# Kernel optimization log

Measured on AMD Instinct MI355X. Metric: run time of the kernel, lower is better.

The kernel has to match this reference:

```python
import jax, jax.numpy as jnp
import numpy as np

NEG_INF = -1.0e9  # matches torch masked_fill value


def setup_inputs() -> dict:
    key = jax.random.key(0)
    k1, k2, k3, k4 = jax.random.split(key, 4)
    B, S, H = 32, 4096, 1024
    query = jax.random.normal(k1, (B, 1, H), dtype=jnp.float32)
    keys = jax.random.normal(k2, (B, S, H), dtype=jnp.float32)
    src_mask = jax.random.randint(k3, (B, S), 0, 2) == 1
    # nn.Linear weight [out,in]; y = x @ W.T
    W_query = jax.random.normal(k4, (H, H), dtype=jnp.float32) * (1.0 / np.sqrt(H))
    return {"query": query, "keys": keys, "src_mask": src_mask, "W_query": W_query}


def reference(query, keys, src_mask, W_query):
    # projected query: [B,1,H] @ W.T -> [B,1,H]
    q = jnp.einsum("bqh,oh->bqo", query, W_query)
    # scores: [B,S] (single query squeezed)
    scores = jnp.einsum("bqh,bsh->bqs", q, keys)[:, 0, :]
    scores = jnp.where(src_mask, NEG_INF, scores)
    weights = jax.nn.softmax(scores, axis=-1)[:, None, :]  # [B,1,S]
    context = jnp.einsum("bqs,bsh->bqh", weights, keys)    # [B,1,H]
    return (context, weights)
```

## Files before the change

### kernel.cpp

```cpp
#include <hip/hip_runtime.h>
#include <math.h>

#define BB 32
#define SS 4096
#define HH 1024
#define NCHUNK 32
#define CHUNK (SS / NCHUNK)
#define NEG_INF9 (-1.0e9f)

__device__ __forceinline__ float wave_reduce_sum(float v) {
#pragma unroll
    for (int off = 32; off > 0; off >>= 1) v += __shfl_xor(v, off, 64);
    return v;
}

__device__ __forceinline__ void wave_reduce_sum2(float& a, float& b) {
#pragma unroll
    for (int off = 32; off > 0; off >>= 1) {
        const float ta = __shfl_xor(a, off, 64);
        const float tb = __shfl_xor(b, off, 64);
        a += ta;
        b += tb;
    }
}

__global__ __launch_bounds__(256) void qproj_kernel(const float* __restrict__ query,
                                                    const float* __restrict__ W,
                                                    float* __restrict__ q) {
    const int b    = blockIdx.y;
    const int wave = threadIdx.x >> 6;
    const int lane = threadIdx.x & 63;

    const float4* qp = (const float4*)(query + (size_t)b * HH);
    float4 qv[4];
#pragma unroll
    for (int r = 0; r < 4; ++r) qv[r] = qp[r * 64 + lane];

    const int obase = blockIdx.x * 64 + wave * 16;
    for (int i = 0; i < 16; ++i) {
        const int o = obase + i;
        const float4* wp = (const float4*)(W + (size_t)o * HH);
        float acc = 0.f;
#pragma unroll
        for (int r = 0; r < 4; ++r) {
            const float4 wv = wp[r * 64 + lane];
            acc += wv.x * qv[r].x + wv.y * qv[r].y + wv.z * qv[r].z + wv.w * qv[r].w;
        }
        acc = wave_reduce_sum(acc);
        if (lane == 0) q[(size_t)b * HH + o] = acc;
    }
}

__global__ __launch_bounds__(256) void attn_chunk_kernel(const float* __restrict__ q,
                                                         const float* __restrict__ keys,
                                                         const int* __restrict__ mask,
                                                         float* __restrict__ raw_scores,
                                                         float* __restrict__ pm,
                                                         float* __restrict__ pl,
                                                         float* __restrict__ pO) {
    const int b    = blockIdx.y;
    const int c    = blockIdx.x;
    const int wave = threadIdx.x >> 6;
    const int lane = threadIdx.x & 63;

    const float4* qp = (const float4*)(q + (size_t)b * HH);
    float4 qv[4];
#pragma unroll
    for (int r = 0; r < 4; ++r) qv[r] = qp[r * 64 + lane];

    float m = -INFINITY;
    float l = 0.f;
    float4 acc[4];
#pragma unroll
    for (int r = 0; r < 4; ++r) acc[r] = make_float4(0.f, 0.f, 0.f, 0.f);

    const size_t bbase = (size_t)b * SS;
    const int s0 = c * CHUNK + wave * 2;

#pragma unroll 4
    for (int i = 0; i < CHUNK / 8; ++i) {
        const int s = s0 + 8 * i;
        const float4* kp0 = (const float4*)(keys + (bbase + s) * HH);
        const float4* kp1 = (const float4*)(keys + (bbase + s + 1) * HH);
        float4 kva[4], kvb[4];
#pragma unroll
        for (int r = 0; r < 4; ++r) { kva[r] = kp0[r * 64 + lane]; kvb[r] = kp1[r * 64 + lane]; }

        float sc0 = 0.f, sc1 = 0.f;
#pragma unroll
        for (int r = 0; r < 4; ++r) {
            sc0 += kva[r].x * qv[r].x + kva[r].y * qv[r].y + kva[r].z * qv[r].z + kva[r].w * qv[r].w;
            sc1 += kvb[r].x * qv[r].x + kvb[r].y * qv[r].y + kvb[r].z * qv[r].z + kvb[r].w * qv[r].w;
        }
        wave_reduce_sum2(sc0, sc1);

        const int2 mk = *(const int2*)(mask + bbase + s);
        if (mk.x != 0) sc0 = NEG_INF9;
        if (mk.y != 0) sc1 = NEG_INF9;
        if (lane == 0) *(float2*)(raw_scores + bbase + s) = make_float2(sc0, sc1);

        const float mnew  = fmaxf(m, fmaxf(sc0, sc1));
        const float scale = __expf(m - mnew);
        const float p0    = __expf(sc0 - mnew);
        const float p1    = __expf(sc1 - mnew);
        l = l * scale + p0 + p1;
#pragma unroll
        for (int r = 0; r < 4; ++r) {
            acc[r].x = acc[r].x * scale + p0 * kva[r].x + p1 * kvb[r].x;
            acc[r].y = acc[r].y * scale + p0 * kva[r].y + p1 * kvb[r].y;
            acc[r].z = acc[r].z * scale + p0 * kva[r].z + p1 * kvb[r].z;
            acc[r].w = acc[r].w * scale + p0 * kva[r].w + p1 * kvb[r].w;
        }
        m = mnew;
    }

    __shared__ float  sm[4];
    __shared__ float  sl[4];
    __shared__ float4 sO[4][256];
#pragma unroll
    for (int r = 0; r < 4; ++r) sO[wave][r * 64 + lane] = acc[r];
    if (lane == 0) { sm[wave] = m; sl[wave] = l; }
    __syncthreads();

    const float M = fmaxf(fmaxf(sm[0], sm[1]), fmaxf(sm[2], sm[3]));
    float f[4];
#pragma unroll
    for (int w = 0; w < 4; ++w) f[w] = __expf(sm[w] - M);
    const float L = sl[0] * f[0] + sl[1] * f[1] + sl[2] * f[2] + sl[3] * f[3];

    const int tid = threadIdx.x;
    float4 o = make_float4(0.f, 0.f, 0.f, 0.f);
#pragma unroll
    for (int w = 0; w < 4; ++w) {
        const float4 v = sO[w][tid];
        o.x += f[w] * v.x; o.y += f[w] * v.y; o.z += f[w] * v.z; o.w += f[w] * v.w;
    }
    ((float4*)(pO + ((size_t)b * NCHUNK + c) * HH))[tid] = o;
    if (tid == 0) { pm[b * NCHUNK + c] = M; pl[b * NCHUNK + c] = L; }
}

__global__ __launch_bounds__(256) void combine_kernel(const float* __restrict__ pm,
                                                      const float* __restrict__ pl,
                                                      const float* __restrict__ pO,
                                                      float* __restrict__ context,
                                                      float* __restrict__ weights) {
    const int b   = blockIdx.x;
    const int tid = threadIdx.x;

    float M = -INFINITY;
#pragma unroll
    for (int c = 0; c < NCHUNK; ++c) M = fmaxf(M, pm[b * NCHUNK + c]);
    float fc[NCHUNK];
    float L = 0.f;
#pragma unroll
    for (int c = 0; c < NCHUNK; ++c) {
        fc[c] = __expf(pm[b * NCHUNK + c] - M);
        L += pl[b * NCHUNK + c] * fc[c];
    }
    const float invL = 1.f / L;

    float4 o = make_float4(0.f, 0.f, 0.f, 0.f);
#pragma unroll
    for (int c = 0; c < NCHUNK; ++c) {
        const float4 v = ((const float4*)(pO + ((size_t)b * NCHUNK + c) * HH))[tid];
        const float g = fc[c] * invL;
        o.x += g * v.x; o.y += g * v.y; o.z += g * v.z; o.w += g * v.w;
    }
    ((float4*)(context + (size_t)b * HH))[tid] = o;

    for (int s = tid; s < SS; s += 256) {
        const float sc = weights[(size_t)b * SS + s];
        weights[(size_t)b * SS + s] = __expf(sc - M) * invL;
    }
}

extern "C" void kernel_launch(void* const* d_in, const int* in_sizes, int n_in,
                              void* d_out, int out_size, void* d_ws, size_t ws_size,
                              hipStream_t stream) {
    const float* query = (const float*)d_in[0];
    const float* keys  = (const float*)d_in[1];
    const int*   mask  = (const int*)d_in[2];
    const float* W     = (const float*)d_in[3];

    float* context = (float*)d_out;
    float* weights = (float*)d_out + (size_t)BB * HH;

    float* q  = (float*)d_ws;
    float* pm = q + (size_t)BB * HH;
    float* pl = pm + BB * NCHUNK;
    float* pO = pl + BB * NCHUNK;

    qproj_kernel<<<dim3(HH / 64, BB), 256, 0, stream>>>(query, W, q);
    attn_chunk_kernel<<<dim3(NCHUNK, BB), 256, 0, stream>>>(q, keys, mask, weights, pm, pl, pO);
    combine_kernel<<<BB, 256, 0, stream>>>(pm, pl, pO, context, weights);
}
```

Baseline: 708.1 us.

## Double-buffer key loads, DPP reductions, more chunks, split combine kernel

The attention kernel now register double-buffers the next pair of key rows and mask values while computing the current pair, and skips the accumulator rescale when the running max does not change. Wave reductions use DPP row operations plus readlane instead of shuffle chains. The chunk count doubles, giving more blocks to fill the GPU, and the combine kernel is split across four blocks per batch to parallelise the context and weight normalisation. The cost is higher register pressure from the double buffer and a larger partial-output workspace. The loop is also fully unrolled.

```diff
diff --git a/kernel.cpp b/kernel.cpp
--- a/kernel.cpp
+++ b/kernel.cpp
@@ -4,24 +4,26 @@
 #define BB 32
 #define SS 4096
 #define HH 1024
-#define NCHUNK 32
+#define NCHUNK 64
 #define CHUNK (SS / NCHUNK)
+#define NSPLIT 4
 #define NEG_INF9 (-1.0e9f)
 
-__device__ __forceinline__ float wave_reduce_sum(float v) {
-#pragma unroll
-    for (int off = 32; off > 0; off >>= 1) v += __shfl_xor(v, off, 64);
-    return v;
-}
-
-__device__ __forceinline__ void wave_reduce_sum2(float& a, float& b) {
-#pragma unroll
-    for (int off = 32; off > 0; off >>= 1) {
-        const float ta = __shfl_xor(a, off, 64);
-        const float tb = __shfl_xor(b, off, 64);
-        a += ta;
-        b += tb;
-    }
+__device__ __forceinline__ float dpp_allreduce_add(float x) {
+    int t;
+    t = __builtin_amdgcn_update_dpp(0, __float_as_int(x), 0x111, 0xf, 0xf, false);
+    x += __int_as_float(t);
+    t = __builtin_amdgcn_update_dpp(0, __float_as_int(x), 0x112, 0xf, 0xf, false);
+    x += __int_as_float(t);
+    t = __builtin_amdgcn_update_dpp(0, __float_as_int(x), 0x114, 0xf, 0xf, false);
+    x += __int_as_float(t);
+    t = __builtin_amdgcn_update_dpp(0, __float_as_int(x), 0x118, 0xf, 0xf, false);
+    x += __int_as_float(t);
+    t = __builtin_amdgcn_update_dpp(0, __float_as_int(x), 0x142, 0xf, 0xf, false);
+    x += __int_as_float(t);
+    t = __builtin_amdgcn_update_dpp(0, __float_as_int(x), 0x143, 0xf, 0xf, false);
+    x += __int_as_float(t);
+    return __int_as_float(__builtin_amdgcn_readlane(__float_as_int(x), 63));
 }
 
 __global__ __launch_bounds__(256) void qproj_kernel(const float* __restrict__ query,
@@ -46,8 +48,8 @@
             const float4 wv = wp[r * 64 + lane];
             acc += wv.x * qv[r].x + wv.y * qv[r].y + wv.z * qv[r].z + wv.w * qv[r].w;
         }
-        acc = wave_reduce_sum(acc);
-        if (lane == 0) q[(size_t)b * HH + o] = acc;
+        const float s = dpp_allreduce_add(acc);
+        if (lane == 0) q[(size_t)b * HH + o] = s;
     }
 }
 
@@ -68,50 +70,73 @@
 #pragma unroll
     for (int r = 0; r < 4; ++r) qv[r] = qp[r * 64 + lane];
 
+    const size_t bbase = (size_t)b * SS;
+    const int s0 = c * CHUNK + wave * 2;
+    const float4* kbase = (const float4*)(keys + (bbase + s0) * HH) + lane;
+
+    float4 ka[2][4], kb[2][4];
+    int2   mk[2];
+
+    {
+        const float4* p0 = kbase;
+        const float4* p1 = kbase + 256;
+#pragma unroll
+        for (int r = 0; r < 4; ++r) { ka[0][r] = p0[r * 64]; kb[0][r] = p1[r * 64]; }
+        mk[0] = *(const int2*)(mask + bbase + s0);
+    }
+
     float m = -INFINITY;
     float l = 0.f;
     float4 acc[4];
 #pragma unroll
     for (int r = 0; r < 4; ++r) acc[r] = make_float4(0.f, 0.f, 0.f, 0.f);
 
-    const size_t bbase = (size_t)b * SS;
-    const int s0 = c * CHUNK + wave * 2;
-
-#pragma unroll 4
+#pragma unroll
     for (int i = 0; i < CHUNK / 8; ++i) {
-        const int s = s0 + 8 * i;
-        const float4* kp0 = (const float4*)(keys + (bbase + s) * HH);
-        const float4* kp1 = (const float4*)(keys + (bbase + s + 1) * HH);
-        float4 kva[4], kvb[4];
-#pragma unroll
-        for (int r = 0; r < 4; ++r) { kva[r] = kp0[r * 64 + lane]; kvb[r] = kp1[r * 64 + lane]; }
-
-        float sc0 = 0.f, sc1 = 0.f;
+        const int cur = i & 1, nxt = cur ^ 1;
+        if (i + 1 < CHUNK / 8) {
+            const float4* p0 = kbase + (size_t)(i + 1) * 8 * 256;
+            const float4* p1 = p0 + 256;
+#pragma unroll
+            for (int r = 0; r < 4; ++r) { ka[nxt][r] = p0[r * 64]; kb[nxt][r] = p1[r * 64]; }
+            mk[nxt] = *(const int2*)(mask + bbase + s0 + 8 * (i + 1));
+        }
+
+        float x0 = 0.f, x1 = 0.f;
 #pragma unroll
         for (int r = 0; r < 4; ++r) {
-            sc0 += kva[r].x * qv[r].x + kva[r].y * qv[r].y + kva[r].z * qv[r].z + kva[r].w * qv[r].w;
-            sc1 += kvb[r].x * qv[r].x + kvb[r].y * qv[r].y + kvb[r].z * qv[r].z + kvb[r].w * qv[r].w;
-        }
-        wave_reduce_sum2(sc0, sc1);
-
-        const int2 mk = *(const int2*)(mask + bbase + s);
-        if (mk.x != 0) sc0 = NEG_INF9;
-        if (mk.y != 0) sc1 = NEG_INF9;
-        if (lane == 0) *(float2*)(raw_scores + bbase + s) = make_float2(sc0, sc1);
-
-        const float mnew  = fmaxf(m, fmaxf(sc0, sc1));
-        const float scale = __expf(m - mnew);
-        const float p0    = __expf(sc0 - mnew);
-        const float p1    = __expf(sc1 - mnew);
-        l = l * scale + p0 + p1;
+            x0 += ka[cur][r].x * qv[r].x + ka[cur][r].y * qv[r].y + ka[cur][r].z * qv[r].z + ka[cur][r].w * qv[r].w;
+            x1 += kb[cur][r].x * qv[r].x + kb[cur][r].y * qv[r].y + kb[cur][r].z * qv[r].z + kb[cur][r].w * qv[r].w;
+        }
+        float sc0 = dpp_allreduce_add(x0);
+        float sc1 = dpp_allreduce_add(x1);
+
+        const int mx = __builtin_amdgcn_readfirstlane(mk[cur].x);
+        const int my = __builtin_amdgcn_readfirstlane(mk[cur].y);
+        if (mx != 0) sc0 = NEG_INF9;
+        if (my != 0) sc1 = NEG_INF9;
+        if (lane == 0) *(float2*)(raw_scores + bbase + s0 + 8 * i) = make_float2(sc0, sc1);
+
+        const float mnew = fmaxf(m, fmaxf(sc0, sc1));
+        if (mnew > m) {
+            const float scale = __expf(m - mnew);
+            l *= scale;
+#pragma unroll
+            for (int r = 0; r < 4; ++r) {
+                acc[r].x *= scale; acc[r].y *= scale; acc[r].z *= scale; acc[r].w *= scale;
+            }
+            m = mnew;
+        }
+        const float p0 = __expf(sc0 - m);
+        const float p1 = __expf(sc1 - m);
+        l += p0 + p1;
 #pragma unroll
         for (int r = 0; r < 4; ++r) {
-            acc[r].x = acc[r].x * scale + p0 * kva[r].x + p1 * kvb[r].x;
-            acc[r].y = acc[r].y * scale + p0 * kva[r].y + p1 * kvb[r].y;
-            acc[r].z = acc[r].z * scale + p0 * kva[r].z + p1 * kvb[r].z;
-            acc[r].w = acc[r].w * scale + p0 * kva[r].w + p1 * kvb[r].w;
-        }
-        m = mnew;
+            acc[r].x += p0 * ka[cur][r].x + p1 * kb[cur][r].x;
+            acc[r].y += p0 * ka[cur][r].y + p1 * kb[cur][r].y;
+            acc[r].z += p0 * ka[cur][r].z + p1 * kb[cur][r].z;
+            acc[r].w += p0 * ka[cur][r].w + p1 * kb[cur][r].w;
+        }
     }
 
     __shared__ float  sm[4];
@@ -144,31 +169,27 @@
                                                       const float* __restrict__ pO,
                                                       float* __restrict__ context,
                                                       float* __restrict__ weights) {
-    const int b   = blockIdx.x;
-    const int tid = threadIdx.x;
+    const int b    = blockIdx.y;
+    const int part = blockIdx.x;
+    const int tid  = threadIdx.x;
 
     float M = -INFINITY;
-#pragma unroll
-    for (int c = 0; c < NCHUNK; ++c) M = fmaxf(M, pm[b * NCHUNK + c]);
-    float fc[NCHUNK];
+#pragma unroll 8
+    for (int cc = 0; cc < NCHUNK; ++cc) M = fmaxf(M, pm[b * NCHUNK + cc]);
     float L = 0.f;
-#pragma unroll
-    for (int c = 0; c < NCHUNK; ++c) {
-        fc[c] = __expf(pm[b * NCHUNK + c] - M);
-        L += pl[b * NCHUNK + c] * fc[c];
-    }
+#pragma unroll 8
+    for (int cc = 0; cc < NCHUNK; ++cc) L += pl[b * NCHUNK + cc] * __expf(pm[b * NCHUNK + cc] - M);
     const float invL = 1.f / L;
 
-    float4 o = make_float4(0.f, 0.f, 0.f, 0.f);
-#pragma unroll
-    for (int c = 0; c < NCHUNK; ++c) {
-        const float4 v = ((const float4*)(pO + ((size_t)b * NCHUNK + c) * HH))[tid];
-        const float g = fc[c] * invL;
-        o.x += g * v.x; o.y += g * v.y; o.z += g * v.z; o.w += g * v.w;
-    }
-    ((float4*)(context + (size_t)b * HH))[tid] = o;
-
-    for (int s = tid; s < SS; s += 256) {
+    const int h = part * 256 + tid;
+    float o = 0.f;
+#pragma unroll 8
+    for (int cc = 0; cc < NCHUNK; ++cc)
+        o += __expf(pm[b * NCHUNK + cc] - M) * pO[((size_t)b * NCHUNK + cc) * HH + h];
+    context[(size_t)b * HH + h] = o * invL;
+
+    const int sbeg = part * (SS / NSPLIT);
+    for (int s = sbeg + tid; s < sbeg + SS / NSPLIT; s += 256) {
         const float sc = weights[(size_t)b * SS + s];
         weights[(size_t)b * SS + s] = __expf(sc - M) * invL;
     }
@@ -192,5 +213,5 @@
 
     qproj_kernel<<<dim3(HH / 64, BB), 256, 0, stream>>>(query, W, q);
     attn_chunk_kernel<<<dim3(NCHUNK, BB), 256, 0, stream>>>(q, keys, mask, weights, pm, pl, pO);
-    combine_kernel<<<BB, 256, 0, stream>>>(pm, pl, pO, context, weights);
-}
+    combine_kernel<<<dim3(NSPLIT, BB), 256, 0, stream>>>(pm, pl, pO, context, weights);
+}
```

Result: no change. 704.8 us (-0.5%).
